# Kernel tuning notes

Measured on AMD Instinct MI355X. Metric: run time of the kernel, lower is better.

Reference implementation:

```python
import jax, jax.numpy as jnp
import numpy as np

EMBED = 1024
HEADS = 16
HEAD_DIM = EMBED // HEADS


def setup_inputs() -> dict:
    key = jax.random.key(0)
    ks = jax.random.split(key, 7)
    B, Sd, Se = 4, 2048, 2048
    dec = jax.random.normal(ks[0], (B, Sd, EMBED), dtype=jnp.float32)
    enc = jax.random.normal(ks[1], (B, Se, EMBED), dtype=jnp.float32)
    scale = 1.0 / np.sqrt(EMBED)
    W_q = jax.random.normal(ks[2], (EMBED, EMBED), dtype=jnp.float32) * scale
    W_k = jax.random.normal(ks[3], (EMBED, EMBED), dtype=jnp.float32) * scale
    W_v = jax.random.normal(ks[4], (EMBED, EMBED), dtype=jnp.float32) * scale
    W_o = jax.random.normal(ks[5], (EMBED, EMBED), dtype=jnp.float32) * scale
    b_o = jax.random.normal(ks[6], (EMBED,), dtype=jnp.float32) * 0.01
    return {"decoder_input": dec, "encoder_output": enc,
            "W_q": W_q, "W_k": W_k, "W_v": W_v, "W_o": W_o, "b_o": b_o}


def reference(decoder_input, encoder_output, W_q, W_k, W_v, W_o, b_o):
    B, Sd, E = decoder_input.shape
    Se = encoder_output.shape[1]
    # projections (nn.Linear applies x @ W.T; here W is stored as [in, out])
    Q = (decoder_input @ W_q).reshape(B, Sd, HEADS, HEAD_DIM)
    K = (encoder_output @ W_k).reshape(B, Se, HEADS, HEAD_DIM)
    V = (encoder_output @ W_v).reshape(B, Se, HEADS, HEAD_DIM)
    # scores: [B, H, Sd, Se]
    scores = jnp.einsum('bqhd,bkhd->bhqk', Q, K) / jnp.sqrt(jnp.float32(HEAD_DIM))
    attn = jax.nn.softmax(scores, axis=-1)
    out = jnp.einsum('bhqk,bkhd->bqhd', attn, V).reshape(B, Sd, E)
    return out @ W_o + b_o
```

## Files before the change

### kernel.cpp

```cpp
#include <hip/hip_runtime.h>
#include <hip/hip_bf16.h>

namespace {

typedef __attribute__((ext_vector_type(8))) short bf16x8;
typedef __attribute__((ext_vector_type(4))) float f32x4;
typedef __attribute__((ext_vector_type(4))) unsigned u32x4v;

constexpr int BATCH = 4;
constexpr int SEQ   = 2048;
constexpr int EMB   = 1024;
constexpr int NH    = 16;
constexpr int HD    = 64;
constexpr int MTOT  = BATCH * SEQ;
constexpr int KVW   = 2 * EMB;
constexpr float LOG2E = 1.44269504088896f;
constexpr float SOFTMAX_C = 16.0f;

__device__ __forceinline__ unsigned short f2bf(float x) {
    unsigned int u = __float_as_uint(x);
    u += 0x7fffu + ((u >> 16) & 1u);
    return (unsigned short)(u >> 16);
}

__device__ __forceinline__ void gl_lds16(const void* g, void* l) {
    __builtin_amdgcn_global_load_lds(
        (const __attribute__((address_space(1))) unsigned int*)g,
        (__attribute__((address_space(3))) unsigned int*)l, 16, 0, 0);
}

__global__ __launch_bounds__(256)
void conv_bf16(const float* __restrict__ dec, const float* __restrict__ enc,
               unsigned short* __restrict__ decb, unsigned short* __restrict__ encb,
               int n4)
{
    int i = blockIdx.x * 256 + threadIdx.x;
    if (i >= n4) return;
    const float* src = blockIdx.y ? enc : dec;
    unsigned short* dst = blockIdx.y ? encb : decb;
    float4 v = ((const float4*)src)[i];
    ushort4 o;
    o.x = f2bf(v.x); o.y = f2bf(v.y); o.z = f2bf(v.z); o.w = f2bf(v.w);
    ((ushort4*)dst)[i] = o;
}

__global__ __launch_bounds__(256)
void wtrans(const float* __restrict__ W0, const float* __restrict__ W1,
            const float* __restrict__ W2, const float* __restrict__ W3,
            unsigned short* __restrict__ WtBase, float qscale)
{
    __shared__ __align__(16) unsigned short Ts[64][65];
    const int tid = threadIdx.x;
    const int z = blockIdx.z;
    const float* W = (z == 0) ? W0 : (z == 1) ? W1 : (z == 2) ? W2 : W3;
    unsigned short* Wt = WtBase + (size_t)z * EMB * EMB;
    const float scale = (z == 0) ? qscale : 1.0f;
    const int n0 = blockIdx.x * 64, k0 = blockIdx.y * 64;
    #pragma unroll
    for (int i = 0; i < 4; ++i) {
        int id = tid + i * 256;
        int r = id >> 4, q = id & 15;
        float4 v = *(const float4*)&W[(size_t)(k0 + r) * EMB + n0 + q * 4];
        Ts[q * 4 + 0][r] = f2bf(v.x * scale);
        Ts[q * 4 + 1][r] = f2bf(v.y * scale);
        Ts[q * 4 + 2][r] = f2bf(v.z * scale);
        Ts[q * 4 + 3][r] = f2bf(v.w * scale);
    }
    __syncthreads();
    #pragma unroll
    for (int i = 0; i < 4; ++i) {
        int id = tid + i * 256;
        int rn = id >> 4, q = id & 15;
        ushort4 o;
        o.x = Ts[rn][q * 4 + 0]; o.y = Ts[rn][q * 4 + 1];
        o.z = Ts[rn][q * 4 + 2]; o.w = Ts[rn][q * 4 + 3];
        *(ushort4*)&Wt[(size_t)(n0 + rn) * EMB + k0 + q * 4] = o;
    }
}

__global__ __launch_bounds__(256)
void vtrans(const unsigned short* __restrict__ V, unsigned short* __restrict__ Vt)
{
    __shared__ __align__(16) unsigned short Ts[64][72];
    const int tid = threadIdx.x;
    const int s0 = blockIdx.x * 64;
    const int bh = blockIdx.y, b = bh >> 4, h = bh & 15;
    #pragma unroll
    for (int it = 0; it < 2; ++it) {
        int id = tid + it * 256;
        int r = id >> 3, seg = id & 7;
        uint4 v = *(const uint4*)&V[(size_t)(b * SEQ + s0 + r) * KVW + h * HD + seg * 8];
        const unsigned short* pv = (const unsigned short*)&v;
        #pragma unroll
        for (int j = 0; j < 8; ++j) Ts[seg * 8 + j][r] = pv[j];
    }
    __syncthreads();
    #pragma unroll
    for (int it = 0; it < 2; ++it) {
        int id = tid + it * 256;
        int d = id >> 3, sg = id & 7;
        int base = (sg >> 2) * 32 + (sg & 3) * 4;
        uint2 wlo = *(const uint2*)&Ts[d][base];
        uint2 whi = *(const uint2*)&Ts[d][base + 16];
        uint4 w;
        w.x = wlo.x; w.y = wlo.y; w.z = whi.x; w.w = whi.y;
        *(uint4*)&Vt[((size_t)bh * HD + d) * SEQ + s0 + sg * 8] = w;
    }
}

template<bool OUT_BF16, bool BIAS>
__device__ __forceinline__
void gemm_body(const unsigned short* __restrict__ A, const unsigned short* __restrict__ Bt,
               const float* __restrict__ bias, void* __restrict__ Cout,
               int m0, int n0, int N, int Kd)
{
    __shared__ __align__(16) unsigned short As[2][128 * 32];
    __shared__ __align__(16) unsigned short Bs[2][128 * 32];
    const int tid  = threadIdx.x;
    const int lane = tid & 63, wave = tid >> 6;
    const int g = lane >> 4, c = lane & 15;
    const int wm = (wave & 1) * 64, wn = (wave >> 1) * 64;

    const int r0 = tid >> 2, s = tid & 3;
    const int sg = s ^ ((r0 + (r0 >> 2)) & 3);
    const unsigned short* ga0 = A  + (size_t)(m0 + r0)      * Kd + sg * 8;
    const unsigned short* ga1 = A  + (size_t)(m0 + r0 + 64) * Kd + sg * 8;
    const unsigned short* gb0 = Bt + (size_t)(n0 + r0)      * Kd + sg * 8;
    const unsigned short* gb1 = Bt + (size_t)(n0 + r0 + 64) * Kd + sg * 8;
    const int lo0 = tid * 8, lo1 = (256 + tid) * 8;

    const int cs = (c + (c >> 2)) & 3;

    f32x4 acc[4][4];
    #pragma unroll
    for (int i = 0; i < 4; ++i)
        #pragma unroll
        for (int j = 0; j < 4; ++j) acc[i][j] = (f32x4)0.0f;

    gl_lds16(ga0, &As[0][lo0]); gl_lds16(ga1, &As[0][lo1]);
    gl_lds16(gb0, &Bs[0][lo0]); gl_lds16(gb1, &Bs[0][lo1]);
    ga0 += 32; ga1 += 32; gb0 += 32; gb1 += 32;
    __syncthreads();

    const int KT = Kd / 32;
    for (int kt = 0; kt < KT; kt += 2) {
        #pragma unroll
        for (int h2 = 0; h2 < 2; ++h2) {
            const int k = kt + h2;
            if (k + 1 < KT) {
                gl_lds16(ga0, &As[h2 ^ 1][lo0]); gl_lds16(ga1, &As[h2 ^ 1][lo1]);
                gl_lds16(gb0, &Bs[h2 ^ 1][lo0]); gl_lds16(gb1, &Bs[h2 ^ 1][lo1]);
                ga0 += 32; ga1 += 32; gb0 += 32; gb1 += 32;
            }
            bf16x8 af[4], bfr[4];
            #pragma unroll
            for (int mt = 0; mt < 4; ++mt)
                af[mt]  = *(const bf16x8*)&As[h2][(wm + mt * 16 + c) * 32 + (g ^ cs) * 8];
            #pragma unroll
            for (int nt = 0; nt < 4; ++nt)
                bfr[nt] = *(const bf16x8*)&Bs[h2][(wn + nt * 16 + c) * 32 + (g ^ cs) * 8];
            #pragma unroll
            for (int mt = 0; mt < 4; ++mt)
                #pragma unroll
                for (int nt = 0; nt < 4; ++nt)
                    acc[mt][nt] = __builtin_amdgcn_mfma_f32_16x16x32_bf16(af[mt], bfr[nt], acc[mt][nt], 0, 0, 0);
            __syncthreads();
        }
    }

    #pragma unroll
    for (int mt = 0; mt < 4; ++mt) {
        #pragma unroll
        for (int nt = 0; nt < 4; ++nt) {
            int n = n0 + wn + nt * 16 + c;
            float bv = BIAS ? bias[n] : 0.0f;
            #pragma unroll
            for (int r = 0; r < 4; ++r) {
                int m = m0 + wm + mt * 16 + 4 * g + r;
                float v = acc[mt][nt][r] + bv;
                if (OUT_BF16) ((unsigned short*)Cout)[(size_t)m * N + n] = f2bf(v);
                else          ((float*)Cout)[(size_t)m * N + n] = v;
            }
        }
    }
}

__global__ __launch_bounds__(256)
void proj_fused(const unsigned short* __restrict__ decb, const unsigned short* __restrict__ encb,
                const unsigned short* __restrict__ WtBase,
                unsigned short* __restrict__ Qb, unsigned short* __restrict__ KVb)
{
    const int fid = blockIdx.y * 24 + blockIdx.x;
    const int xcd = fid & 7, idx = fid >> 3;
    const int mt  = (xcd << 3) | (idx / 24);
    const int nt  = idx % 24;
    const int m0  = mt * 128;
    if (nt < 8) {
        gemm_body<true, false>(decb, WtBase, nullptr, Qb, m0, nt * 128, EMB, EMB);
    } else {
        gemm_body<true, false>(encb, WtBase + (size_t)EMB * EMB, nullptr, KVb,
                               m0, (nt - 8) * 128, KVW, EMB);
    }
}

__global__ __launch_bounds__(256)
void proj_out(const unsigned short* __restrict__ Ob, const unsigned short* __restrict__ WoT,
              const float* __restrict__ bo, float* __restrict__ out)
{
    const int fid = blockIdx.y * 8 + blockIdx.x;
    const int xcd = fid & 7, idx = fid >> 3;
    const int mt  = (xcd << 3) | (idx >> 3);
    const int nt  = idx & 7;
    gemm_body<false, true>(Ob, WoT, bo, out, mt * 128, nt * 128, EMB, EMB);
}

__global__ __launch_bounds__(256)
void attn(const unsigned short* __restrict__ Q, const unsigned short* __restrict__ KV,
          const unsigned short* __restrict__ Vt, unsigned short* __restrict__ O)
{
    __shared__ __align__(16) unsigned short Ks[2][64 * 64];
    __shared__ __align__(16) unsigned short Vs[2][64 * 64];

    const int tid  = threadIdx.x;
    const int lane = tid & 63, wave = tid >> 6;
    const int g = lane >> 4, c = lane & 15, c7 = c & 7;

    const int fid  = blockIdx.y * 16 + blockIdx.x;
    const int xcd  = fid & 7, idx = fid >> 3;
    const int bh   = (xcd << 3) | (idx >> 4);
    const int qblk = idx & 15;
    const int b = bh >> 4, h = bh & 15;
    const int qw = qblk * 128 + wave * 32;

    const unsigned short* Qp0 = Q + (size_t)(b * SEQ + qw + c) * EMB + h * HD;
    const unsigned short* Qp1 = Qp0 + (size_t)16 * EMB;
    bf16x8 qb[2][2];
    qb[0][0] = *(const bf16x8*)(Qp0 + g * 8);
    qb[0][1] = *(const bf16x8*)(Qp0 + 32 + g * 8);
    qb[1][0] = *(const bf16x8*)(Qp1 + g * 8);
    qb[1][1] = *(const bf16x8*)(Qp1 + 32 + g * 8);

    const int r0 = tid >> 3, s8 = tid & 7;
    const int sg = s8 ^ (r0 & 7);
    const unsigned short* gK0 = KV + ((size_t)b * SEQ + r0) * KVW + h * HD + sg * 8;
    const unsigned short* gK1 = gK0 + (size_t)32 * KVW;
    const unsigned short* gV0 = Vt + (size_t)bh * HD * SEQ + (size_t)r0 * SEQ + sg * 8;
    const unsigned short* gV1 = gV0 + (size_t)32 * SEQ;
    const int lo0 = tid * 8, lo1 = (256 + tid) * 8;

    f32x4 oac[2][4];
    #pragma unroll
    for (int bd = 0; bd < 2; ++bd)
        #pragma unroll
        for (int dt = 0; dt < 4; ++dt) oac[bd][dt] = (f32x4)0.0f;
    float lrun[2] = {0.0f, 0.0f};
    const f32x4 minit = {-SOFTMAX_C, -SOFTMAX_C, -SOFTMAX_C, -SOFTMAX_C};

    gl_lds16(gK0, &Ks[0][lo0]); gl_lds16(gK1, &Ks[0][lo1]);
    gl_lds16(gV0, &Vs[0][lo0]); gl_lds16(gV1, &Vs[0][lo1]);
    gK0 += (size_t)64 * KVW; gK1 += (size_t)64 * KVW; gV0 += 64; gV1 += 64;
    __syncthreads();

    constexpr int T = SEQ / 64;
    for (int t = 0; t < T; t += 2) {
        #pragma unroll
        for (int h2 = 0; h2 < 2; ++h2) {
            const int tt = t + h2;
            if (tt + 1 < T) {
                gl_lds16(gK0, &Ks[h2 ^ 1][lo0]); gl_lds16(gK1, &Ks[h2 ^ 1][lo1]);
                gl_lds16(gV0, &Vs[h2 ^ 1][lo0]); gl_lds16(gV1, &Vs[h2 ^ 1][lo1]);
                gK0 += (size_t)64 * KVW; gK1 += (size_t)64 * KVW;
                gV0 += 64;               gV1 += 64;
            }

            f32x4 st[2][4];
            __builtin_amdgcn_s_setprio(1);
            #pragma unroll
            for (int kt = 0; kt < 4; ++kt) {
                bf16x8 ka0 = *(const bf16x8*)&Ks[h2][(kt * 16 + c) * 64 + (g ^ c7) * 8];
                bf16x8 ka1 = *(const bf16x8*)&Ks[h2][(kt * 16 + c) * 64 + ((4 + g) ^ c7) * 8];
                #pragma unroll
                for (int bd = 0; bd < 2; ++bd) {
                    st[bd][kt] = __builtin_amdgcn_mfma_f32_16x16x32_bf16(ka0, qb[bd][0], minit, 0, 0, 0);
                    st[bd][kt] = __builtin_amdgcn_mfma_f32_16x16x32_bf16(ka1, qb[bd][1], st[bd][kt], 0, 0, 0);
                }
            }
            __builtin_amdgcn_s_setprio(0);

            bf16x8 pa[2][2];
            #pragma unroll
            for (int bd = 0; bd < 2; ++bd) {
                float ls = lrun[bd];
                unsigned uu[8];
                #pragma unroll
                for (int kt = 0; kt < 4; ++kt) {
                    float p0 = __builtin_amdgcn_exp2f(st[bd][kt][0]);
                    float p1 = __builtin_amdgcn_exp2f(st[bd][kt][1]);
                    float p2 = __builtin_amdgcn_exp2f(st[bd][kt][2]);
                    float p3 = __builtin_amdgcn_exp2f(st[bd][kt][3]);
                    ls += (p0 + p1) + (p2 + p3);
                    asm("v_cvt_pk_bf16_f32 %0, %1, %2" : "=v"(uu[2 * kt])     : "v"(p0), "v"(p1));
                    asm("v_cvt_pk_bf16_f32 %0, %1, %2" : "=v"(uu[2 * kt + 1]) : "v"(p2), "v"(p3));
                }
                lrun[bd] = ls;
                u32x4v w0 = {uu[0], uu[1], uu[2], uu[3]};
                u32x4v w1 = {uu[4], uu[5], uu[6], uu[7]};
                pa[bd][0] = __builtin_bit_cast(bf16x8, w0);
                pa[bd][1] = __builtin_bit_cast(bf16x8, w1);
            }

            __builtin_amdgcn_s_setprio(1);
            #pragma unroll
            for (int dt = 0; dt < 4; ++dt) {
                bf16x8 vb0 = *(const bf16x8*)&Vs[h2][(dt * 16 + c) * 64 + (g ^ c7) * 8];
                bf16x8 vb1 = *(const bf16x8*)&Vs[h2][(dt * 16 + c) * 64 + ((4 + g) ^ c7) * 8];
                #pragma unroll
                for (int bd = 0; bd < 2; ++bd) {
                    oac[bd][dt] = __builtin_amdgcn_mfma_f32_16x16x32_bf16(pa[bd][0], vb0, oac[bd][dt], 0, 0, 0);
                    oac[bd][dt] = __builtin_amdgcn_mfma_f32_16x16x32_bf16(pa[bd][1], vb1, oac[bd][dt], 0, 0, 0);
                }
            }
            __builtin_amdgcn_s_setprio(0);

            __syncthreads();
        }
    }

    #pragma unroll
    for (int bd = 0; bd < 2; ++bd) {
        float v = lrun[bd];
        v += __shfl_xor(v, 16);
        v += __shfl_xor(v, 32);
        lrun[bd] = v;
    }
    #pragma unroll
    for (int bd = 0; bd < 2; ++bd) {
        unsigned short* Op = O + (size_t)(b * SEQ + qw + bd * 16) * EMB + h * HD;
        #pragma unroll
        for (int r = 0; r < 4; ++r) {
            float linv = 1.0f / __shfl(lrun[bd], 4 * g + r);
            #pragma unroll
            for (int dt = 0; dt < 4; ++dt)
                Op[(size_t)(4 * g + r) * EMB + dt * 16 + c] = f2bf(oac[bd][dt][r] * linv);
        }
    }
}

}

extern "C" void kernel_launch(void* const* d_in, const int* in_sizes, int n_in,
                              void* d_out, int out_size, void* d_ws, size_t ws_size,
                              hipStream_t stream)
{
    const float* dec = (const float*)d_in[0];
    const float* enc = (const float*)d_in[1];
    const float* Wq  = (const float*)d_in[2];
    const float* Wk  = (const float*)d_in[3];
    const float* Wv  = (const float*)d_in[4];
    const float* Wo  = (const float*)d_in[5];
    const float* bo  = (const float*)d_in[6];
    float* out = (float*)d_out;

    const size_t BIG = (size_t)MTOT * EMB;
    const size_t SML = (size_t)EMB * EMB;
    unsigned short* decb = (unsigned short*)d_ws;
    unsigned short* encb = decb + BIG;
    unsigned short* WqT  = encb + BIG;
    unsigned short* WoT  = WqT + 3 * SML;
    unsigned short* Qb   = WqT + 4 * SML;
    unsigned short* KVb  = Qb + BIG;
    unsigned short* Vtg  = KVb + 2 * BIG;
    unsigned short* Ob   = Vtg + BIG;

    dim3 blk(256);

    conv_bf16<<<dim3((unsigned)(BIG / 4 / 256), 2), blk, 0, stream>>>(
        dec, enc, decb, encb, (int)(BIG / 4));

    wtrans<<<dim3(16, 16, 4), blk, 0, stream>>>(Wq, Wk, Wv, Wo, WqT, 0.125f * LOG2E);

    proj_fused<<<dim3(24, MTOT / 128), blk, 0, stream>>>(decb, encb, WqT, Qb, KVb);

    vtrans<<<dim3(SEQ / 64, BATCH * NH), blk, 0, stream>>>(KVb + EMB, Vtg);

    attn<<<dim3(SEQ / 128, BATCH * NH), blk, 0, stream>>>(Qb, KVb, Vtg, Ob);

    proj_out<<<dim3(EMB / 128, MTOT / 128), blk, 0, stream>>>(Ob, WoT, bo, out);
}
```

Baseline: 308.5 us.

## Merge prep kernels and compute softmax row sums with MFMA against ones

Combines the fp32-to-bf16 activation conversion and the weight transpose into one launch by splitting work on blockIdx.z. This saves a kernel launch and the gap between launches, but leaves many idle blocks in the weight slice that exit early. In the attention loop, the per-lane scalar accumulation of exponentials is replaced with extra MFMAs that multiply the bf16 probability tiles by a vector of ones. That removes VALU adds and the final cross-lane shuffles, at the cost of more matrix-core work and row sums taken from bf16-rounded probabilities.

```diff
diff --git a/kernel.cpp b/kernel.cpp
--- a/kernel.cpp
+++ b/kernel.cpp
@@ -30,32 +30,31 @@
 }
 
 __global__ __launch_bounds__(256)
-void conv_bf16(const float* __restrict__ dec, const float* __restrict__ enc,
-               unsigned short* __restrict__ decb, unsigned short* __restrict__ encb,
-               int n4)
-{
-    int i = blockIdx.x * 256 + threadIdx.x;
-    if (i >= n4) return;
-    const float* src = blockIdx.y ? enc : dec;
-    unsigned short* dst = blockIdx.y ? encb : decb;
-    float4 v = ((const float4*)src)[i];
-    ushort4 o;
-    o.x = f2bf(v.x); o.y = f2bf(v.y); o.z = f2bf(v.z); o.w = f2bf(v.w);
-    ((ushort4*)dst)[i] = o;
-}
-
-__global__ __launch_bounds__(256)
-void wtrans(const float* __restrict__ W0, const float* __restrict__ W1,
-            const float* __restrict__ W2, const float* __restrict__ W3,
-            unsigned short* __restrict__ WtBase, float qscale)
+void prep(const float* __restrict__ dec, const float* __restrict__ enc,
+          unsigned short* __restrict__ decb, unsigned short* __restrict__ encb, int n4,
+          const float* __restrict__ W0, const float* __restrict__ W1,
+          const float* __restrict__ W2, const float* __restrict__ W3,
+          unsigned short* __restrict__ WtBase, float qscale)
 {
     __shared__ __align__(16) unsigned short Ts[64][65];
     const int tid = threadIdx.x;
-    const int z = blockIdx.z;
+    if (blockIdx.z < 2) {
+        int i = blockIdx.x * 256 + tid;
+        if (i >= n4) return;
+        const float* src = blockIdx.z ? enc : dec;
+        unsigned short* dst = blockIdx.z ? encb : decb;
+        float4 v = ((const float4*)src)[i];
+        ushort4 o;
+        o.x = f2bf(v.x); o.y = f2bf(v.y); o.z = f2bf(v.z); o.w = f2bf(v.w);
+        ((ushort4*)dst)[i] = o;
+        return;
+    }
+    if (blockIdx.x >= 1024) return;
+    const int z = blockIdx.x >> 8;
     const float* W = (z == 0) ? W0 : (z == 1) ? W1 : (z == 2) ? W2 : W3;
     unsigned short* Wt = WtBase + (size_t)z * EMB * EMB;
     const float scale = (z == 0) ? qscale : 1.0f;
-    const int n0 = blockIdx.x * 64, k0 = blockIdx.y * 64;
+    const int n0 = (blockIdx.x & 15) * 64, k0 = ((blockIdx.x >> 4) & 15) * 64;
     #pragma unroll
     for (int i = 0; i < 4; ++i) {
         int id = tid + i * 256;
@@ -253,8 +252,11 @@
     for (int bd = 0; bd < 2; ++bd)
         #pragma unroll
         for (int dt = 0; dt < 4; ++dt) oac[bd][dt] = (f32x4)0.0f;
-    float lrun[2] = {0.0f, 0.0f};
+    f32x4 lacc[2];
+    lacc[0] = (f32x4)0.0f; lacc[1] = (f32x4)0.0f;
     const f32x4 minit = {-SOFTMAX_C, -SOFTMAX_C, -SOFTMAX_C, -SOFTMAX_C};
+    const short onebf = (short)0x3F80;
+    const bf16x8 vones = {onebf, onebf, onebf, onebf, onebf, onebf, onebf, onebf};
 
     gl_lds16(gK0, &Ks[0][lo0]); gl_lds16(gK1, &Ks[0][lo1]);
     gl_lds16(gV0, &Vs[0][lo0]); gl_lds16(gV1, &Vs[0][lo1]);
@@ -290,7 +292,6 @@
             bf16x8 pa[2][2];
             #pragma unroll
             for (int bd = 0; bd < 2; ++bd) {
-                float ls = lrun[bd];
                 unsigned uu[8];
                 #pragma unroll
                 for (int kt = 0; kt < 4; ++kt) {
@@ -298,11 +299,9 @@
                     float p1 = __builtin_amdgcn_exp2f(st[bd][kt][1]);
                     float p2 = __builtin_amdgcn_exp2f(st[bd][kt][2]);
                     float p3 = __builtin_amdgcn_exp2f(st[bd][kt][3]);
-                    ls += (p0 + p1) + (p2 + p3);
                     asm("v_cvt_pk_bf16_f32 %0, %1, %2" : "=v"(uu[2 * kt])     : "v"(p0), "v"(p1));
                     asm("v_cvt_pk_bf16_f32 %0, %1, %2" : "=v"(uu[2 * kt + 1]) : "v"(p2), "v"(p3));
                 }
-                lrun[bd] = ls;
                 u32x4v w0 = {uu[0], uu[1], uu[2], uu[3]};
                 u32x4v w1 = {uu[4], uu[5], uu[6], uu[7]};
                 pa[bd][0] = __builtin_bit_cast(bf16x8, w0);
@@ -320,6 +319,11 @@
                     oac[bd][dt] = __builtin_amdgcn_mfma_f32_16x16x32_bf16(pa[bd][1], vb1, oac[bd][dt], 0, 0, 0);
                 }
             }
+            #pragma unroll
+            for (int bd = 0; bd < 2; ++bd) {
+                lacc[bd] = __builtin_amdgcn_mfma_f32_16x16x32_bf16(pa[bd][0], vones, lacc[bd], 0, 0, 0);
+                lacc[bd] = __builtin_amdgcn_mfma_f32_16x16x32_bf16(pa[bd][1], vones, lacc[bd], 0, 0, 0);
+            }
             __builtin_amdgcn_s_setprio(0);
 
             __syncthreads();
@@ -328,17 +332,10 @@
 
     #pragma unroll
     for (int bd = 0; bd < 2; ++bd) {
-        float v = lrun[bd];
-        v += __shfl_xor(v, 16);
-        v += __shfl_xor(v, 32);
-        lrun[bd] = v;
-    }
-    #pragma unroll
-    for (int bd = 0; bd < 2; ++bd) {
         unsigned short* Op = O + (size_t)(b * SEQ + qw + bd * 16) * EMB + h * HD;
         #pragma unroll
         for (int r = 0; r < 4; ++r) {
-            float linv = 1.0f / __shfl(lrun[bd], 4 * g + r);
+            float linv = 1.0f / lacc[bd][r];
             #pragma unroll
             for (int dt = 0; dt < 4; ++dt)
                 Op[(size_t)(4 * g + r) * EMB + dt * 16 + c] = f2bf(oac[bd][dt][r] * linv);
@@ -374,10 +371,9 @@
 
     dim3 blk(256);
 
-    conv_bf16<<<dim3((unsigned)(BIG / 4 / 256), 2), blk, 0, stream>>>(
-        dec, enc, decb, encb, (int)(BIG / 4));
-
-    wtrans<<<dim3(16, 16, 4), blk, 0, stream>>>(Wq, Wk, Wv, Wo, WqT, 0.125f * LOG2E);
+    prep<<<dim3((unsigned)(BIG / 4 / 256), 1, 3), blk, 0, stream>>>(
+        dec, enc, decb, encb, (int)(BIG / 4),
+        Wq, Wk, Wv, Wo, WqT, 0.125f * LOG2E);
 
     proj_fused<<<dim3(24, MTOT / 128), blk, 0, stream>>>(decb, encb, WqT, Qb, KVb);
 
```

After: 323.6 us. +4.9%, slower.

## Halve attention query tile per block and compute row sums via MFMA

Applied to the files above, without the earlier changes.

Each attention block now handles 64 query rows (16 per wave) instead of 128, which doubles the grid and halves per-wave MFMA work and register use. The softmax row-sum is now accumulated with an extra MFMA against a ones vector instead of scalar adds plus cross-lane shuffles. Occupancy and parallelism should rise, but each block reloads K and V for fewer queries, so K/V memory traffic doubles.

```diff
diff --git a/kernel.cpp b/kernel.cpp
--- a/kernel.cpp
+++ b/kernel.cpp
@@ -225,20 +225,17 @@
     const int lane = tid & 63, wave = tid >> 6;
     const int g = lane >> 4, c = lane & 15, c7 = c & 7;
 
-    const int fid  = blockIdx.y * 16 + blockIdx.x;
+    const int fid  = blockIdx.y * 32 + blockIdx.x;
     const int xcd  = fid & 7, idx = fid >> 3;
-    const int bh   = (xcd << 3) | (idx >> 4);
-    const int qblk = idx & 15;
+    const int bh   = (xcd << 3) | (idx >> 5);
+    const int qblk = idx & 31;
     const int b = bh >> 4, h = bh & 15;
-    const int qw = qblk * 128 + wave * 32;
+    const int qw = qblk * 64 + wave * 16;
 
     const unsigned short* Qp0 = Q + (size_t)(b * SEQ + qw + c) * EMB + h * HD;
-    const unsigned short* Qp1 = Qp0 + (size_t)16 * EMB;
-    bf16x8 qb[2][2];
-    qb[0][0] = *(const bf16x8*)(Qp0 + g * 8);
-    qb[0][1] = *(const bf16x8*)(Qp0 + 32 + g * 8);
-    qb[1][0] = *(const bf16x8*)(Qp1 + g * 8);
-    qb[1][1] = *(const bf16x8*)(Qp1 + 32 + g * 8);
+    bf16x8 qb[2];
+    qb[0] = *(const bf16x8*)(Qp0 + g * 8);
+    qb[1] = *(const bf16x8*)(Qp0 + 32 + g * 8);
 
     const int r0 = tid >> 3, s8 = tid & 7;
     const int sg = s8 ^ (r0 & 7);
@@ -248,13 +245,13 @@
     const unsigned short* gV1 = gV0 + (size_t)32 * SEQ;
     const int lo0 = tid * 8, lo1 = (256 + tid) * 8;
 
-    f32x4 oac[2][4];
-    #pragma unroll
-    for (int bd = 0; bd < 2; ++bd)
-        #pragma unroll
-        for (int dt = 0; dt < 4; ++dt) oac[bd][dt] = (f32x4)0.0f;
-    float lrun[2] = {0.0f, 0.0f};
+    f32x4 oac[4];
+    #pragma unroll
+    for (int dt = 0; dt < 4; ++dt) oac[dt] = (f32x4)0.0f;
+    f32x4 lacc = (f32x4)0.0f;
     const f32x4 minit = {-SOFTMAX_C, -SOFTMAX_C, -SOFTMAX_C, -SOFTMAX_C};
+    const short onebf = (short)0x3F80;
+    const bf16x8 vones = {onebf, onebf, onebf, onebf, onebf, onebf, onebf, onebf};
 
     gl_lds16(gK0, &Ks[0][lo0]); gl_lds16(gK1, &Ks[0][lo1]);
     gl_lds16(gV0, &Vs[0][lo0]); gl_lds16(gV1, &Vs[0][lo1]);
@@ -273,40 +270,33 @@
                 gV0 += 64;               gV1 += 64;
             }
 
-            f32x4 st[2][4];
+            f32x4 st[4];
             __builtin_amdgcn_s_setprio(1);
             #pragma unroll
             for (int kt = 0; kt < 4; ++kt) {
                 bf16x8 ka0 = *(const bf16x8*)&Ks[h2][(kt * 16 + c) * 64 + (g ^ c7) * 8];
                 bf16x8 ka1 = *(const bf16x8*)&Ks[h2][(kt * 16 + c) * 64 + ((4 + g) ^ c7) * 8];
-                #pragma unroll
-                for (int bd = 0; bd < 2; ++bd) {
-                    st[bd][kt] = __builtin_amdgcn_mfma_f32_16x16x32_bf16(ka0, qb[bd][0], minit, 0, 0, 0);
-                    st[bd][kt] = __builtin_amdgcn_mfma_f32_16x16x32_bf16(ka1, qb[bd][1], st[bd][kt], 0, 0, 0);
-                }
+                st[kt] = __builtin_amdgcn_mfma_f32_16x16x32_bf16(ka0, qb[0], minit, 0, 0, 0);
+                st[kt] = __builtin_amdgcn_mfma_f32_16x16x32_bf16(ka1, qb[1], st[kt], 0, 0, 0);
             }
             __builtin_amdgcn_s_setprio(0);
 
-            bf16x8 pa[2][2];
-            #pragma unroll
-            for (int bd = 0; bd < 2; ++bd) {
-                float ls = lrun[bd];
+            bf16x8 pa[2];
+            {
                 unsigned uu[8];
                 #pragma unroll
                 for (int kt = 0; kt < 4; ++kt) {
-                    float p0 = __builtin_amdgcn_exp2f(st[bd][kt][0]);
-                    float p1 = __builtin_amdgcn_exp2f(st[bd][kt][1]);
-                    float p2 = __builtin_amdgcn_exp2f(st[bd][kt][2]);
-                    float p3 = __builtin_amdgcn_exp2f(st[bd][kt][3]);
-                    ls += (p0 + p1) + (p2 + p3);
+                    float p0 = __builtin_amdgcn_exp2f(st[kt][0]);
+                    float p1 = __builtin_amdgcn_exp2f(st[kt][1]);
+                    float p2 = __builtin_amdgcn_exp2f(st[kt][2]);
+                    float p3 = __builtin_amdgcn_exp2f(st[kt][3]);
                     asm("v_cvt_pk_bf16_f32 %0, %1, %2" : "=v"(uu[2 * kt])     : "v"(p0), "v"(p1));
                     asm("v_cvt_pk_bf16_f32 %0, %1, %2" : "=v"(uu[2 * kt + 1]) : "v"(p2), "v"(p3));
                 }
-                lrun[bd] = ls;
                 u32x4v w0 = {uu[0], uu[1], uu[2], uu[3]};
                 u32x4v w1 = {uu[4], uu[5], uu[6], uu[7]};
-                pa[bd][0] = __builtin_bit_cast(bf16x8, w0);
-                pa[bd][1] = __builtin_bit_cast(bf16x8, w1);
+                pa[0] = __builtin_bit_cast(bf16x8, w0);
+                pa[1] = __builtin_bit_cast(bf16x8, w1);
             }
 
             __builtin_amdgcn_s_setprio(1);
@@ -314,35 +304,24 @@
             for (int dt = 0; dt < 4; ++dt) {
                 bf16x8 vb0 = *(const bf16x8*)&Vs[h2][(dt * 16 + c) * 64 + (g ^ c7) * 8];
                 bf16x8 vb1 = *(const bf16x8*)&Vs[h2][(dt * 16 + c) * 64 + ((4 + g) ^ c7) * 8];
-                #pragma unroll
-                for (int bd = 0; bd < 2; ++bd) {
-                    oac[bd][dt] = __builtin_amdgcn_mfma_f32_16x16x32_bf16(pa[bd][0], vb0, oac[bd][dt], 0, 0, 0);
-                    oac[bd][dt] = __builtin_amdgcn_mfma_f32_16x16x32_bf16(pa[bd][1], vb1, oac[bd][dt], 0, 0, 0);
-                }
-            }
+                oac[dt] = __builtin_amdgcn_mfma_f32_16x16x32_bf16(pa[0], vb0, oac[dt], 0, 0, 0);
+                oac[dt] = __builtin_amdgcn_mfma_f32_16x16x32_bf16(pa[1], vb1, oac[dt], 0, 0, 0);
+            }
+            lacc = __builtin_amdgcn_mfma_f32_16x16x32_bf16(pa[0], vones, lacc, 0, 0, 0);
+            lacc = __builtin_amdgcn_mfma_f32_16x16x32_bf16(pa[1], vones, lacc, 0, 0, 0);
             __builtin_amdgcn_s_setprio(0);
 
             __syncthreads();
         }
     }
 
-    #pragma unroll
-    for (int bd = 0; bd < 2; ++bd) {
-        float v = lrun[bd];
-        v += __shfl_xor(v, 16);
-        v += __shfl_xor(v, 32);
-        lrun[bd] = v;
-    }
-    #pragma unroll
-    for (int bd = 0; bd < 2; ++bd) {
-        unsigned short* Op = O + (size_t)(b * SEQ + qw + bd * 16) * EMB + h * HD;
-        #pragma unroll
-        for (int r = 0; r < 4; ++r) {
-            float linv = 1.0f / __shfl(lrun[bd], 4 * g + r);
-            #pragma unroll
-            for (int dt = 0; dt < 4; ++dt)
-                Op[(size_t)(4 * g + r) * EMB + dt * 16 + c] = f2bf(oac[bd][dt][r] * linv);
-        }
+    unsigned short* Op = O + (size_t)(b * SEQ + qw) * EMB + h * HD;
+    #pragma unroll
+    for (int r = 0; r < 4; ++r) {
+        float linv = 1.0f / lacc[r];
+        #pragma unroll
+        for (int dt = 0; dt < 4; ++dt)
+            Op[(size_t)(4 * g + r) * EMB + dt * 16 + c] = f2bf(oac[dt][r] * linv);
     }
 }
 
@@ -383,7 +362,7 @@
 
     vtrans<<<dim3(SEQ / 64, BATCH * NH), blk, 0, stream>>>(KVb + EMB, Vtg);
 
-    attn<<<dim3(SEQ / 128, BATCH * NH), blk, 0, stream>>>(Qb, KVb, Vtg, Ob);
+    attn<<<dim3(SEQ / 64, BATCH * NH), blk, 0, stream>>>(Qb, KVb, Vtg, Ob);
 
     proj_out<<<dim3(EMB / 128, MTOT / 128), blk, 0, stream>>>(Ob, WoT, bo, out);
 }
```

Measured after the change: 315.2 us. 2.1% more time.
